# Optimization experiments

Hardware: AMD Instinct MI355X
Metric: run time of the kernel (lower is better)

The kernel has to match this reference:

```python
import jax, jax.numpy as jnp
from jax import lax
import numpy as np

F_IN, F_OUT, T = 32, 64, 8
H1 = (3 * F_IN + F_OUT) // 4  # 40
H2 = F_OUT                    # 64
N, E = 50000, 800000


def setup_inputs() -> dict:
    key = jax.random.key(0)
    ks = jax.random.split(key, 8)
    def p(k, shape, fan_in):
        return jax.random.normal(k, shape, jnp.float32) / np.float32(np.sqrt(fan_in))
    return {
        "temporal_features": jax.random.normal(ks[0], (N, F_IN, T), jnp.float32),
        "src": jax.random.randint(ks[1], (E,), 0, N, jnp.int32),
        "dst": jax.random.randint(ks[2], (E,), 0, N, jnp.int32),
        "W1": p(ks[3], (F_IN, H1), F_IN), "b1": jnp.zeros((H1,), jnp.float32),
        "W2": p(ks[4], (H1, H2), H1),   "b2": jnp.zeros((H2,), jnp.float32),
        "W3": p(ks[5], (H2, F_OUT), H2), "b3": jnp.zeros((F_OUT,), jnp.float32),
        "Wc": p(ks[6], (F_OUT, F_OUT, 3), F_OUT * 3),  # Conv1d weight [out, in, k]
        "bc": jnp.zeros((F_OUT,), jnp.float32),
    }


def _graph_conv(h, src, dst, out_norm, in_norm, W, b, act, n):
    # dgl GraphConv, norm='both': D_out^{-1/2} -> sum-aggregate -> D_in^{-1/2} -> linear
    h = h * out_norm[:, None, None]                       # [N, t, f]
    agg = jax.ops.segment_sum(h[src], dst, num_segments=n)  # irregular gather/scatter
    h = agg * in_norm[:, None, None]
    h = jnp.einsum("nti,io->nto", h, W) + b
    return jax.nn.relu(h) if act else h


def reference(temporal_features, src, dst, W1, b1, W2, b2, W3, b3, Wc, bc):
    n = temporal_features.shape[0]
    ones = jnp.ones(src.shape, temporal_features.dtype)
    out_deg = jax.ops.segment_sum(ones, src, num_segments=n)
    in_deg = jax.ops.segment_sum(ones, dst, num_segments=n)
    out_norm = jnp.clip(out_deg, 1.0, None) ** -0.5
    in_norm = jnp.clip(in_deg, 1.0, None) ** -0.5

    h = jnp.swapaxes(temporal_features, -2, -1)  # [N, t, f_in]
    h = _graph_conv(h, src, dst, out_norm, in_norm, W1, b1, True, n)
    h = _graph_conv(h, src, dst, out_norm, in_norm, W2, b2, True, n)
    h = _graph_conv(h, src, dst, out_norm, in_norm, W3, b3, False, n)
    h = jnp.swapaxes(h, -2, -1)  # [N, f_out, t]

    out = lax.conv_general_dilated(
        h, Wc, window_strides=(1,), padding=((1, 1),),
        dimension_numbers=("NCH", "OIH", "NCH"))
    return out + bc[None, :, None]
```

## Files before the change

kernel.cpp:

```cpp
#include <hip/hip_runtime.h>


__global__ __launch_bounds__(256) void deg_kernel(const int* __restrict__ src,
                                                  const int* __restrict__ dst,
                                                  int* __restrict__ out_deg,
                                                  int* __restrict__ in_deg, int E) {
  int e = blockIdx.x * 256 + threadIdx.x;
  if (e < E) {
    atomicAdd(&out_deg[src[e]], 1);
    atomicAdd(&in_deg[dst[e]], 1);
  }
}

__global__ __launch_bounds__(256) void norm_kernel(const int* __restrict__ out_deg,
                                                   const int* __restrict__ in_deg,
                                                   float* __restrict__ out_norm,
                                                   float* __restrict__ in_norm, int N) {
  int n = blockIdx.x * 256 + threadIdx.x;
  if (n < N) {
    out_norm[n] = 1.0f / sqrtf((float)max(out_deg[n], 1));
    in_norm[n]  = 1.0f / sqrtf((float)max(in_deg[n], 1));
  }
}

__global__ __launch_bounds__(256) void wct_kernel(const float* __restrict__ Wc,
                                                  float* __restrict__ wct) {
  int m = blockIdx.x * 256 + threadIdx.x;
  if (m < 12288) wct[m] = Wc[(m & 63) * 192 + (m >> 6)];
}


__global__ __launch_bounds__(256) void scan_partial_kernel(const int* __restrict__ deg,
                                                           int* __restrict__ partial, int N) {
  __shared__ int ws[4];
  int tid = threadIdx.x, lane = tid & 63, wv = tid >> 6;
  int base = blockIdx.x * 1024;
  int v = 0;
#pragma unroll
  for (int k = 0; k < 4; ++k) {
    int i = base + tid + k * 256;
    if (i < N) v += deg[i];
  }
  for (int d = 32; d > 0; d >>= 1) v += __shfl_down(v, d, 64);
  if (lane == 0) ws[wv] = v;
  __syncthreads();
  if (tid == 0) partial[blockIdx.x] = ws[0] + ws[1] + ws[2] + ws[3];
}

__global__ __launch_bounds__(1024) void scan_partials_kernel(int* __restrict__ partial, int P) {
  __shared__ int wsum[16];
  int tid = threadIdx.x, lane = tid & 63, wv = tid >> 6;
  int v = (tid < P) ? partial[tid] : 0;
  int x = v;
  for (int d = 1; d < 64; d <<= 1) {
    int y = __shfl_up(x, d, 64);
    if (lane >= d) x += y;
  }
  if (lane == 63) wsum[wv] = x;
  __syncthreads();
  if (wv == 0 && lane < 16) {
    int y = wsum[lane];
    int z = y;
    for (int d = 1; d < 16; d <<= 1) {
      int q = __shfl_up(z, d, 64);
      if (lane >= d) z += q;
    }
    wsum[lane] = z - y;
  }
  __syncthreads();
  if (tid < P) partial[tid] = wsum[wv] + x - v;
}

__global__ __launch_bounds__(1024) void scan_apply_kernel(const int* __restrict__ deg,
                                                          const int* __restrict__ partial,
                                                          int* __restrict__ off, int N) {
  __shared__ int wsum[16];
  int tid = threadIdx.x, lane = tid & 63, wv = tid >> 6;
  int i = blockIdx.x * 1024 + tid;
  int v = (i < N) ? deg[i] : 0;
  int x = v;
  for (int d = 1; d < 64; d <<= 1) {
    int y = __shfl_up(x, d, 64);
    if (lane >= d) x += y;
  }
  if (lane == 63) wsum[wv] = x;
  __syncthreads();
  if (wv == 0 && lane < 16) {
    int y = wsum[lane];
    int z = y;
    for (int d = 1; d < 16; d <<= 1) {
      int q = __shfl_up(z, d, 64);
      if (lane >= d) z += q;
    }
    wsum[lane] = z - y;
  }
  __syncthreads();
  int excl = partial[blockIdx.x] + wsum[wv] + (x - v);
  if (i < N) off[i] = excl;
  if (i == N - 1) off[N] = excl + v;
}

__global__ __launch_bounds__(256) void scatter_kernel(const int* __restrict__ src,
                                                      const int* __restrict__ dst,
                                                      const int* __restrict__ in_off,
                                                      int* __restrict__ cursor,
                                                      int* __restrict__ csr_src, int E) {
  int e = blockIdx.x * 256 + threadIdx.x;
  if (e < E) {
    int d = dst[e];
    int p = atomicAdd(&cursor[d], 1);
    csr_src[in_off[d] + p] = src[e];
  }
}

template <int F_IN, int F_OUT, int TS, int L, bool IT_LAYOUT, bool RELU,
          bool GNORM, bool SCALE_OUT, bool TSTORE>
__device__ __forceinline__ void layer_body(
    const float* __restrict__ h_in, const int* __restrict__ csr_src,
    const int* __restrict__ in_off, const float* __restrict__ out_norm,
    const float* __restrict__ in_norm, const float* __restrict__ W,
    const float* __restrict__ bias, float* __restrict__ h_out, int N) {
  constexpr int NF4 = F_IN * 2;
  constexpr int NC = NF4 / L;
  constexpr int M = 64 / L;
  constexpr int SLOTS = 4 * M;
  constexpr int SLOT = (IT_LAYOUT ? F_IN * 8 : TS * 8) + 8;
  __shared__ float agg[SLOTS][SLOT];
  int tid = threadIdx.x;
  int wave = tid >> 6, lane = tid & 63;
  int q = lane / L, r = lane % L;
  int slot = wave * M + q;
  int n = blockIdx.x * SLOTS + slot;
  bool valid = (n < N);

  float4 acc[NC];
#pragma unroll
  for (int k = 0; k < NC; ++k) acc[k] = make_float4(0.f, 0.f, 0.f, 0.f);

  if (valid) {
    int e0 = in_off[n], e1 = in_off[n + 1];
    const float4* h4 = (const float4*)h_in;
    int j = e0;
    if (e1 - e0 >= 2) {
      int sA = csr_src[j], sB = csr_src[j + 1];
      do {
        int cA = sA, cB = sB;
        int jn = j + 2;
        sA = csr_src[min(jn, e1 - 1)];
        sB = csr_src[min(jn + 1, e1 - 1)];
        float wA = 1.f, wB = 1.f;
        if constexpr (GNORM) { wA = out_norm[cA]; wB = out_norm[cB]; }
        const float4* pA = h4 + (size_t)cA * NF4 + r;
        const float4* pB = h4 + (size_t)cB * NF4 + r;
        float4 vA[NC], vB[NC];
#pragma unroll
        for (int k = 0; k < NC; ++k) vA[k] = pA[k * L];
#pragma unroll
        for (int k = 0; k < NC; ++k) vB[k] = pB[k * L];
#pragma unroll
        for (int k = 0; k < NC; ++k) {
          acc[k].x = fmaf(vA[k].x, wA, acc[k].x);
          acc[k].y = fmaf(vA[k].y, wA, acc[k].y);
          acc[k].z = fmaf(vA[k].z, wA, acc[k].z);
          acc[k].w = fmaf(vA[k].w, wA, acc[k].w);
          acc[k].x = fmaf(vB[k].x, wB, acc[k].x);
          acc[k].y = fmaf(vB[k].y, wB, acc[k].y);
          acc[k].z = fmaf(vB[k].z, wB, acc[k].z);
          acc[k].w = fmaf(vB[k].w, wB, acc[k].w);
        }
        j = jn;
      } while (j + 2 <= e1);
    }
    if (j < e1) {
      int s = csr_src[j];
      float w = 1.f;
      if constexpr (GNORM) w = out_norm[s];
      const float4* p = h4 + (size_t)s * NF4 + r;
#pragma unroll
      for (int k = 0; k < NC; ++k) {
        float4 v = p[k * L];
        acc[k].x = fmaf(v.x, w, acc[k].x);
        acc[k].y = fmaf(v.y, w, acc[k].y);
        acc[k].z = fmaf(v.z, w, acc[k].z);
        acc[k].w = fmaf(v.w, w, acc[k].w);
      }
    }
    float innm = in_norm[n];
#pragma unroll
    for (int k = 0; k < NC; ++k) {
      int el = (k * L + r) * 4;
      int addr;
      if constexpr (IT_LAYOUT) {
        addr = el;
      } else {
        int t = el / F_IN;
        int i = el - t * F_IN;
        addr = t * TS + i;
      }
      *(float4*)&agg[slot][addr] = make_float4(acc[k].x * innm, acc[k].y * innm,
                                               acc[k].z * innm, acc[k].w * innm);
    }
  }
  __syncthreads();

  constexpr int G = F_OUT / 8;
  int t = lane >> 3, og = lane & 7;
  float acc2[M][G];
  {
    float bb[G];
    if constexpr (G == 8) {
      float4 bA = *(const float4*)&bias[og * 8];
      float4 bB = *(const float4*)&bias[og * 8 + 4];
      bb[0] = bA.x; bb[1] = bA.y; bb[2] = bA.z; bb[3] = bA.w;
      bb[4] = bB.x; bb[5] = bB.y; bb[6] = bB.z; bb[7] = bB.w;
    } else {
#pragma unroll
      for (int c = 0; c < G; ++c) bb[c] = bias[og * G + c];
    }
#pragma unroll
    for (int qq = 0; qq < M; ++qq)
#pragma unroll
      for (int c = 0; c < G; ++c) acc2[qq][c] = bb[c];
  }
#pragma unroll 4
  for (int i = 0; i < F_IN; ++i) {
    float wrow[G];
    if constexpr (G == 8) {
      float4 wA = *(const float4*)&W[i * F_OUT + og * 8];
      float4 wB = *(const float4*)&W[i * F_OUT + og * 8 + 4];
      wrow[0] = wA.x; wrow[1] = wA.y; wrow[2] = wA.z; wrow[3] = wA.w;
      wrow[4] = wB.x; wrow[5] = wB.y; wrow[6] = wB.z; wrow[7] = wB.w;
    } else {
#pragma unroll
      for (int c = 0; c < G; ++c) wrow[c] = W[i * F_OUT + og * G + c];
    }
    int raddr;
    if constexpr (IT_LAYOUT) raddr = i * 8 + t;
    else raddr = t * TS + i;
#pragma unroll
    for (int qq = 0; qq < M; ++qq) {
      float a = agg[wave * M + qq][raddr];
#pragma unroll
      for (int c = 0; c < G; ++c) acc2[qq][c] = fmaf(a, wrow[c], acc2[qq][c]);
    }
  }
#pragma unroll
  for (int qq = 0; qq < M; ++qq) {
    int n2 = blockIdx.x * SLOTS + wave * M + qq;
    if (n2 < N) {
      float osc = 1.f;
      if constexpr (SCALE_OUT) osc = out_norm[n2];
      float res[G];
#pragma unroll
      for (int c = 0; c < G; ++c) {
        float v = acc2[qq][c];
        if constexpr (RELU) v = fmaxf(v, 0.f);
        res[c] = v * osc;
      }
      if constexpr (TSTORE) {
        float* ob = h_out + (size_t)n2 * 512 + og * 64 + t;
#pragma unroll
        for (int c = 0; c < G; ++c) ob[c * 8] = res[c];
      } else {
        float* orow = h_out + (size_t)n2 * (F_OUT * 8) + t * F_OUT + og * G;
        if constexpr (G == 8) {
          *(float4*)&orow[0] = make_float4(res[0], res[1], res[2], res[3]);
          *(float4*)&orow[4] = make_float4(res[4], res[5], res[6], res[7]);
        } else {
#pragma unroll
          for (int c = 0; c < G; ++c) orow[c] = res[c];
        }
      }
    }
  }
}

__global__ __launch_bounds__(256) void layer1_k(
    const float* __restrict__ h_in, const int* __restrict__ csr_src,
    const int* __restrict__ in_off, const float* __restrict__ out_norm,
    const float* __restrict__ in_norm, const float* __restrict__ W,
    const float* __restrict__ bias, float* __restrict__ h_out, int N) {
  layer_body<32, 40, 0, 8, true, true, true, true, false>(
      h_in, csr_src, in_off, out_norm, in_norm, W, bias, h_out, N);
}

__global__ __launch_bounds__(256) void layer2_k(
    const float* __restrict__ h_in, const int* __restrict__ csr_src,
    const int* __restrict__ in_off, const float* __restrict__ out_norm,
    const float* __restrict__ in_norm, const float* __restrict__ W,
    const float* __restrict__ bias, float* __restrict__ h_out, int N) {
  layer_body<40, 64, 44, 16, false, true, false, true, false>(
      h_in, csr_src, in_off, out_norm, in_norm, W, bias, h_out, N);
}

__global__ __launch_bounds__(256) void layer3_k(
    const float* __restrict__ h_in, const int* __restrict__ csr_src,
    const int* __restrict__ in_off, const float* __restrict__ out_norm,
    const float* __restrict__ in_norm, const float* __restrict__ W,
    const float* __restrict__ bias, float* __restrict__ h_out, int N) {
  layer_body<64, 64, 68, 16, false, false, false, false, true>(
      h_in, csr_src, in_off, out_norm, in_norm, W, bias, h_out, N);
}

__global__ __launch_bounds__(256) void conv_qn_kernel(const float* __restrict__ wct,
                                                      const float* __restrict__ bc,
                                                      float* dout, int N) {
  __shared__ float hlds[4][4 * 516];
  int tid = threadIdx.x, wave = tid >> 6, lane = tid & 63;
  int q = lane >> 4, r = lane & 15;
  int base = blockIdx.x * 16 + wave * 4;
  float* hl = hlds[wave];

  const float4* g4 = (const float4*)dout;
  long long wb4 = (long long)base * 128;
  long long lim = (long long)N * 128;
#pragma unroll
  for (int k = 0; k < 8; ++k) {
    long long F4 = wb4 + k * 64 + lane;
    float4 v = make_float4(0.f, 0.f, 0.f, 0.f);
    if (F4 < lim) v = g4[F4];
    int local = k * 64 + lane;
    int qp = local >> 7, rem = local & 127;
    *(float4*)&hl[qp * 516 + rem * 4] = v;
  }

  float4 b4 = *(const float4*)&bc[r * 4];
  float bcv[4] = {b4.x, b4.y, b4.z, b4.w};
  float acc[4][8];
#pragma unroll
  for (int c = 0; c < 4; ++c)
#pragma unroll
    for (int t = 0; t < 8; ++t) acc[c][t] = bcv[c];

  const float4* wct4 = (const float4*)wct;
  const float* hq = &hl[q * 516];
#pragma unroll 2
  for (int i = 0; i < 64; ++i) {
    float4 hA = *(const float4*)&hq[i * 8];
    float4 hB = *(const float4*)&hq[i * 8 + 4];
    float4 w0 = wct4[(i * 3 + 0) * 16 + r];
    float4 w1 = wct4[(i * 3 + 1) * 16 + r];
    float4 w2 = wct4[(i * 3 + 2) * 16 + r];
    float h[8] = {hA.x, hA.y, hA.z, hA.w, hB.x, hB.y, hB.z, hB.w};
    float wk0[4] = {w0.x, w0.y, w0.z, w0.w};
    float wk1[4] = {w1.x, w1.y, w1.z, w1.w};
    float wk2[4] = {w2.x, w2.y, w2.z, w2.w};
#pragma unroll
    for (int c = 0; c < 4; ++c) {
#pragma unroll
      for (int t = 0; t < 8; ++t) acc[c][t] = fmaf(wk1[c], h[t], acc[c][t]);
#pragma unroll
      for (int t = 1; t < 8; ++t) acc[c][t] = fmaf(wk0[c], h[t - 1], acc[c][t]);
#pragma unroll
      for (int t = 0; t < 7; ++t) acc[c][t] = fmaf(wk2[c], h[t + 1], acc[c][t]);
    }
  }
  int n = base + q;
  if (n < N) {
    float* ob = dout + (size_t)n * 512 + r * 32;
#pragma unroll
    for (int c = 0; c < 4; ++c) {
      *(float4*)&ob[c * 8] = make_float4(acc[c][0], acc[c][1], acc[c][2], acc[c][3]);
      *(float4*)&ob[c * 8 + 4] = make_float4(acc[c][4], acc[c][5], acc[c][6], acc[c][7]);
    }
  }
}


extern "C" void kernel_launch(void* const* d_in, const int* in_sizes, int n_in,
                              void* d_out, int out_size, void* d_ws, size_t ws_size,
                              hipStream_t stream) {
  const float* tf = (const float*)d_in[0];
  const int* src = (const int*)d_in[1];
  const int* dst = (const int*)d_in[2];
  const float* W1 = (const float*)d_in[3];
  const float* b1 = (const float*)d_in[4];
  const float* W2 = (const float*)d_in[5];
  const float* b2 = (const float*)d_in[6];
  const float* W3 = (const float*)d_in[7];
  const float* b3 = (const float*)d_in[8];
  const float* Wc = (const float*)d_in[9];
  const float* bc = (const float*)d_in[10];

  int N = in_sizes[0] / 256;
  int E = in_sizes[1];

  char* ws = (char*)d_ws;
  size_t pos = 0;
  auto alloc = [&](size_t bytes) -> void* {
    void* p = ws + pos;
    pos += (bytes + 255) & ~(size_t)255;
    return p;
  };
  int* in_deg   = (int*)alloc((size_t)N * 4);
  int* out_deg  = (int*)alloc((size_t)N * 4);
  int* cursor   = (int*)alloc((size_t)N * 4);
  int* in_off   = (int*)alloc((size_t)(N + 1) * 4);
  int* partial  = (int*)alloc((size_t)1024 * 4);
  float* o_norm = (float*)alloc((size_t)N * 4);
  float* i_norm = (float*)alloc((size_t)N * 4);
  int* csr      = (int*)alloc((size_t)E * 4);
  float* wct    = (float*)alloc((size_t)12288 * 4);
  float* h1     = (float*)alloc((size_t)N * 320 * 4);
  float* h2     = (float*)alloc((size_t)N * 512 * 4);
  float* h3     = (float*)d_out;

  hipMemsetAsync(in_deg, 0, (size_t)((char*)in_off - (char*)in_deg), stream);

  deg_kernel<<<(E + 255) / 256, 256, 0, stream>>>(src, dst, out_deg, in_deg, E);
  norm_kernel<<<(N + 255) / 256, 256, 0, stream>>>(out_deg, in_deg, o_norm, i_norm, N);
  wct_kernel<<<48, 256, 0, stream>>>(Wc, wct);

  int P = (N + 1023) / 1024;
  scan_partial_kernel<<<P, 256, 0, stream>>>(in_deg, partial, N);
  scan_partials_kernel<<<1, 1024, 0, stream>>>(partial, P);
  scan_apply_kernel<<<P, 1024, 0, stream>>>(in_deg, partial, in_off, N);

  scatter_kernel<<<(E + 255) / 256, 256, 0, stream>>>(src, dst, in_off, cursor, csr, E);

  layer1_k<<<(N + 31) / 32, 256, 0, stream>>>(tf, csr, in_off, o_norm, i_norm, W1, b1, h1, N);
  layer2_k<<<(N + 15) / 16, 256, 0, stream>>>(h1, csr, in_off, o_norm, i_norm, W2, b2, h2, N);
  layer3_k<<<(N + 15) / 16, 256, 0, stream>>>(h2, csr, in_off, o_norm, i_norm, W3, b3, h3, N);

  conv_qn_kernel<<<(N + 15) / 16, 256, 0, stream>>>(wct, bc, (float*)d_out, N);
}
```

Baseline: 906.6 us.

## Fuse layer-3 graph conv with temporal Conv1d and drop block barriers

Layer 3's aggregation and linear transform are merged with the temporal Conv1d into one kernel. The layer-3 result stays in shared memory with an XOR swizzle instead of going to the output buffer and being read back, which removes one full N×512 global write and read plus a launch. The change also drops the shared-memory padding in the other layers, sets occupancy hints through launch_bounds, and removes __syncthreads. That last part relies on each wave reading only its own slots; any cross-lane LDS reads within a wave now depend on no barrier being needed.

```diff
diff --git a/kernel.cpp b/kernel.cpp
--- a/kernel.cpp
+++ b/kernel.cpp
@@ -114,7 +114,7 @@
 }
 
 template <int F_IN, int F_OUT, int TS, int L, bool IT_LAYOUT, bool RELU,
-          bool GNORM, bool SCALE_OUT, bool TSTORE>
+          bool GNORM, bool SCALE_OUT, int WPE>
 __device__ __forceinline__ void layer_body(
     const float* __restrict__ h_in, const int* __restrict__ csr_src,
     const int* __restrict__ in_off, const float* __restrict__ out_norm,
@@ -124,7 +124,7 @@
   constexpr int NC = NF4 / L;
   constexpr int M = 64 / L;
   constexpr int SLOTS = 4 * M;
-  constexpr int SLOT = (IT_LAYOUT ? F_IN * 8 : TS * 8) + 8;
+  constexpr int SLOT = IT_LAYOUT ? F_IN * 8 : TS * 8;
   __shared__ float agg[SLOTS][SLOT];
   int tid = threadIdx.x;
   int wave = tid >> 6, lane = tid & 63;
@@ -190,7 +190,7 @@
     for (int k = 0; k < NC; ++k) {
       int el = (k * L + r) * 4;
       int addr;
-      if constexpr (IT_LAYOUT) {
+      if constexpr (IT_LAYOUT || TS == F_IN) {
         addr = el;
       } else {
         int t = el / F_IN;
@@ -201,7 +201,6 @@
                                                acc[k].z * innm, acc[k].w * innm);
     }
   }
-  __syncthreads();
 
   constexpr int G = F_OUT / 8;
   int t = lane >> 3, og = lane & 7;
@@ -257,87 +256,149 @@
         if constexpr (RELU) v = fmaxf(v, 0.f);
         res[c] = v * osc;
       }
-      if constexpr (TSTORE) {
-        float* ob = h_out + (size_t)n2 * 512 + og * 64 + t;
-#pragma unroll
-        for (int c = 0; c < G; ++c) ob[c * 8] = res[c];
+      float* orow = h_out + (size_t)n2 * (F_OUT * 8) + t * F_OUT + og * G;
+      if constexpr (G == 8) {
+        *(float4*)&orow[0] = make_float4(res[0], res[1], res[2], res[3]);
+        *(float4*)&orow[4] = make_float4(res[4], res[5], res[6], res[7]);
       } else {
-        float* orow = h_out + (size_t)n2 * (F_OUT * 8) + t * F_OUT + og * G;
-        if constexpr (G == 8) {
-          *(float4*)&orow[0] = make_float4(res[0], res[1], res[2], res[3]);
-          *(float4*)&orow[4] = make_float4(res[4], res[5], res[6], res[7]);
-        } else {
-#pragma unroll
-          for (int c = 0; c < G; ++c) orow[c] = res[c];
-        }
+#pragma unroll
+        for (int c = 0; c < G; ++c) orow[c] = res[c];
       }
     }
   }
 }
 
-__global__ __launch_bounds__(256) void layer1_k(
+__global__ __launch_bounds__(256, 5) void layer1_k(
     const float* __restrict__ h_in, const int* __restrict__ csr_src,
     const int* __restrict__ in_off, const float* __restrict__ out_norm,
     const float* __restrict__ in_norm, const float* __restrict__ W,
     const float* __restrict__ bias, float* __restrict__ h_out, int N) {
-  layer_body<32, 40, 0, 8, true, true, true, true, false>(
+  layer_body<32, 40, 0, 8, true, true, true, true, 5>(
       h_in, csr_src, in_off, out_norm, in_norm, W, bias, h_out, N);
 }
 
-__global__ __launch_bounds__(256) void layer2_k(
+__global__ __launch_bounds__(256, 6) void layer2_k(
     const float* __restrict__ h_in, const int* __restrict__ csr_src,
     const int* __restrict__ in_off, const float* __restrict__ out_norm,
     const float* __restrict__ in_norm, const float* __restrict__ W,
     const float* __restrict__ bias, float* __restrict__ h_out, int N) {
-  layer_body<40, 64, 44, 16, false, true, false, true, false>(
+  layer_body<40, 64, 40, 16, false, true, false, true, 6>(
       h_in, csr_src, in_off, out_norm, in_norm, W, bias, h_out, N);
 }
 
-__global__ __launch_bounds__(256) void layer3_k(
+__global__ __launch_bounds__(256, 4) void layer3_conv_k(
     const float* __restrict__ h_in, const int* __restrict__ csr_src,
-    const int* __restrict__ in_off, const float* __restrict__ out_norm,
-    const float* __restrict__ in_norm, const float* __restrict__ W,
-    const float* __restrict__ bias, float* __restrict__ h_out, int N) {
-  layer_body<64, 64, 68, 16, false, false, false, false, true>(
-      h_in, csr_src, in_off, out_norm, in_norm, W, bias, h_out, N);
-}
-
-__global__ __launch_bounds__(256) void conv_qn_kernel(const float* __restrict__ wct,
-                                                      const float* __restrict__ bc,
-                                                      float* dout, int N) {
-  __shared__ float hlds[4][4 * 516];
-  int tid = threadIdx.x, wave = tid >> 6, lane = tid & 63;
+    const int* __restrict__ in_off, const float* __restrict__ in_norm,
+    const float* __restrict__ W, const float* __restrict__ bias,
+    const float* __restrict__ wct, const float* __restrict__ bc,
+    float* __restrict__ out, int N) {
+  __shared__ float agg[16][512];
+  int tid = threadIdx.x;
+  int wave = tid >> 6, lane = tid & 63;
   int q = lane >> 4, r = lane & 15;
-  int base = blockIdx.x * 16 + wave * 4;
-  float* hl = hlds[wave];
-
-  const float4* g4 = (const float4*)dout;
-  long long wb4 = (long long)base * 128;
-  long long lim = (long long)N * 128;
-#pragma unroll
-  for (int k = 0; k < 8; ++k) {
-    long long F4 = wb4 + k * 64 + lane;
-    float4 v = make_float4(0.f, 0.f, 0.f, 0.f);
-    if (F4 < lim) v = g4[F4];
-    int local = k * 64 + lane;
-    int qp = local >> 7, rem = local & 127;
-    *(float4*)&hl[qp * 516 + rem * 4] = v;
+  int slot = wave * 4 + q;
+  int n = blockIdx.x * 16 + slot;
+  bool valid = (n < N);
+
+  float4 acc[8];
+#pragma unroll
+  for (int k = 0; k < 8; ++k) acc[k] = make_float4(0.f, 0.f, 0.f, 0.f);
+
+  if (valid) {
+    int e0 = in_off[n], e1 = in_off[n + 1];
+    const float4* h4 = (const float4*)h_in;
+    int j = e0;
+    if (e1 - e0 >= 2) {
+      int sA = csr_src[j], sB = csr_src[j + 1];
+      do {
+        int cA = sA, cB = sB;
+        int jn = j + 2;
+        sA = csr_src[min(jn, e1 - 1)];
+        sB = csr_src[min(jn + 1, e1 - 1)];
+        const float4* pA = h4 + (size_t)cA * 128 + r;
+        const float4* pB = h4 + (size_t)cB * 128 + r;
+        float4 vA[8], vB[8];
+#pragma unroll
+        for (int k = 0; k < 8; ++k) vA[k] = pA[k * 16];
+#pragma unroll
+        for (int k = 0; k < 8; ++k) vB[k] = pB[k * 16];
+#pragma unroll
+        for (int k = 0; k < 8; ++k) {
+          acc[k].x += vA[k].x + vB[k].x;
+          acc[k].y += vA[k].y + vB[k].y;
+          acc[k].z += vA[k].z + vB[k].z;
+          acc[k].w += vA[k].w + vB[k].w;
+        }
+        j = jn;
+      } while (j + 2 <= e1);
+    }
+    if (j < e1) {
+      int s = csr_src[j];
+      const float4* p = h4 + (size_t)s * 128 + r;
+#pragma unroll
+      for (int k = 0; k < 8; ++k) {
+        float4 v = p[k * 16];
+        acc[k].x += v.x; acc[k].y += v.y; acc[k].z += v.z; acc[k].w += v.w;
+      }
+    }
+    float innm = in_norm[n];
+#pragma unroll
+    for (int k = 0; k < 8; ++k) {
+      int f4i = k * 16 + (r ^ k);
+      *(float4*)&agg[slot][f4i * 4] = make_float4(acc[k].x * innm, acc[k].y * innm,
+                                                  acc[k].z * innm, acc[k].w * innm);
+    }
+  }
+
+  int t = lane >> 3, og = lane & 7;
+  float acc2[4][8];
+  {
+    float4 bA = *(const float4*)&bias[og * 8];
+    float4 bB = *(const float4*)&bias[og * 8 + 4];
+    float bb[8] = {bA.x, bA.y, bA.z, bA.w, bB.x, bB.y, bB.z, bB.w};
+#pragma unroll
+    for (int qq = 0; qq < 4; ++qq)
+#pragma unroll
+      for (int c = 0; c < 8; ++c) acc2[qq][c] = bb[c];
+  }
+  int tb = t * 64;
+#pragma unroll 4
+  for (int i = 0; i < 64; ++i) {
+    float4 wA = *(const float4*)&W[i * 64 + og * 8];
+    float4 wB = *(const float4*)&W[i * 64 + og * 8 + 4];
+    float wrow[8] = {wA.x, wA.y, wA.z, wA.w, wB.x, wB.y, wB.z, wB.w};
+    int raddr = tb + (((i >> 2) ^ t) << 2) + (i & 3);
+#pragma unroll
+    for (int qq = 0; qq < 4; ++qq) {
+      float a = agg[wave * 4 + qq][raddr];
+#pragma unroll
+      for (int c = 0; c < 8; ++c) acc2[qq][c] = fmaf(a, wrow[c], acc2[qq][c]);
+    }
+  }
+
+#pragma unroll
+  for (int qq = 0; qq < 4; ++qq) {
+    float* sb = &agg[wave * 4 + qq][og * 64 + t];
+#pragma unroll
+    for (int c = 0; c < 8; ++c) sb[(c ^ (og & 3)) << 3] = acc2[qq][c];
   }
 
   float4 b4 = *(const float4*)&bc[r * 4];
   float bcv[4] = {b4.x, b4.y, b4.z, b4.w};
-  float acc[4][8];
+  float cacc[4][8];
 #pragma unroll
   for (int c = 0; c < 4; ++c)
 #pragma unroll
-    for (int t = 0; t < 8; ++t) acc[c][t] = bcv[c];
+    for (int tt = 0; tt < 8; ++tt) cacc[c][tt] = bcv[c];
 
   const float4* wct4 = (const float4*)wct;
-  const float* hq = &hl[q * 516];
+  const float* hq = &agg[wave * 4 + q][0];
 #pragma unroll 2
   for (int i = 0; i < 64; ++i) {
-    float4 hA = *(const float4*)&hq[i * 8];
-    float4 hB = *(const float4*)&hq[i * 8 + 4];
+    int ib = i >> 3, ic = i & 7;
+    const float* hi = &hq[ib * 64 + ((ic ^ (ib & 3)) << 3)];
+    float4 hA = *(const float4*)hi;
+    float4 hB = *(const float4*)(hi + 4);
     float4 w0 = wct4[(i * 3 + 0) * 16 + r];
     float4 w1 = wct4[(i * 3 + 1) * 16 + r];
     float4 w2 = wct4[(i * 3 + 2) * 16 + r];
@@ -348,20 +409,19 @@
 #pragma unroll
     for (int c = 0; c < 4; ++c) {
 #pragma unroll
-      for (int t = 0; t < 8; ++t) acc[c][t] = fmaf(wk1[c], h[t], acc[c][t]);
-#pragma unroll
-      for (int t = 1; t < 8; ++t) acc[c][t] = fmaf(wk0[c], h[t - 1], acc[c][t]);
-#pragma unroll
-      for (int t = 0; t < 7; ++t) acc[c][t] = fmaf(wk2[c], h[t + 1], acc[c][t]);
-    }
-  }
-  int n = base + q;
-  if (n < N) {
-    float* ob = dout + (size_t)n * 512 + r * 32;
+      for (int tt = 0; tt < 8; ++tt) cacc[c][tt] = fmaf(wk1[c], h[tt], cacc[c][tt]);
+#pragma unroll
+      for (int tt = 1; tt < 8; ++tt) cacc[c][tt] = fmaf(wk0[c], h[tt - 1], cacc[c][tt]);
+#pragma unroll
+      for (int tt = 0; tt < 7; ++tt) cacc[c][tt] = fmaf(wk2[c], h[tt + 1], cacc[c][tt]);
+    }
+  }
+  if (valid) {
+    float* ob = out + (size_t)n * 512 + r * 32;
 #pragma unroll
     for (int c = 0; c < 4; ++c) {
-      *(float4*)&ob[c * 8] = make_float4(acc[c][0], acc[c][1], acc[c][2], acc[c][3]);
-      *(float4*)&ob[c * 8 + 4] = make_float4(acc[c][4], acc[c][5], acc[c][6], acc[c][7]);
+      *(float4*)&ob[c * 8] = make_float4(cacc[c][0], cacc[c][1], cacc[c][2], cacc[c][3]);
+      *(float4*)&ob[c * 8 + 4] = make_float4(cacc[c][4], cacc[c][5], cacc[c][6], cacc[c][7]);
     }
   }
 }
@@ -403,7 +463,6 @@
   float* wct    = (float*)alloc((size_t)12288 * 4);
   float* h1     = (float*)alloc((size_t)N * 320 * 4);
   float* h2     = (float*)alloc((size_t)N * 512 * 4);
-  float* h3     = (float*)d_out;
 
   hipMemsetAsync(in_deg, 0, (size_t)((char*)in_off - (char*)in_deg), stream);
 
@@ -420,7 +479,6 @@
 
   layer1_k<<<(N + 31) / 32, 256, 0, stream>>>(tf, csr, in_off, o_norm, i_norm, W1, b1, h1, N);
   layer2_k<<<(N + 15) / 16, 256, 0, stream>>>(h1, csr, in_off, o_norm, i_norm, W2, b2, h2, N);
-  layer3_k<<<(N + 15) / 16, 256, 0, stream>>>(h2, csr, in_off, o_norm, i_norm, W3, b3, h3, N);
-
-  conv_qn_kernel<<<(N + 15) / 16, 256, 0, stream>>>(wct, bc, (float*)d_out, N);
-}
+  layer3_conv_k<<<(N + 15) / 16, 256, 0, stream>>>(h2, csr, in_off, i_norm, W3, b3,
+                                                   wct, bc, (float*)d_out, N);
+}
```

New measurement: 888.0 us. -2.0%, faster.
